# Kernel tuning notes

Hardware: AMD Instinct MI355X
Metric: run time of the kernel (lower is better)

The kernel has to match this reference:

```python
import jax, jax.numpy as jnp
import numpy as np

TAU = 1.1      # LIF membrane time constant
ALPHA = 4.0    # sigmoid surrogate sharpness (spikingjelly default)
EPS = 1e-5     # BatchNorm eps
SCALE = 0.125  # attention scale


def lif(x, v_th):
    # Single-step LIF, v init 0, decay_input=True: v = x / tau; spike = H(v - v_th)
    # Straight-through: forward heaviside, backward sigmoid surrogate derivative.
    u = x / TAU - v_th
    sg = jax.nn.sigmoid(ALPHA * u)
    return sg + jax.lax.stop_gradient((u >= 0.0).astype(x.dtype) - sg)


def bn(x, gamma, beta):
    # BatchNorm1d in training mode on [B, C, N]: stats over (B, N) per channel
    mean = jnp.mean(x, axis=(0, 2), keepdims=True)
    var = jnp.var(x, axis=(0, 2), keepdims=True)
    return gamma[None, :, None] * (x - mean) * jax.lax.rsqrt(var + EPS) + beta[None, :, None]


def conv1x1(w, x):
    # Conv1d kernel_size=1: pointwise channel mix, x: [B,C,N], w: [O,C]
    return jnp.einsum('oc,bcn->bon', w, x)


def setup_inputs() -> dict:
    key = jax.random.key(0)
    B, C, N = 32, 512, 1024
    ks = jax.random.split(key, 6)
    s = 1.0 / np.sqrt(C)
    inp = {"x": jax.random.normal(ks[0], (B, C, N), jnp.float32)}
    for name, k in zip(["q", "k", "v", "proj"], ks[1:5]):
        inp[name + "_w"] = jax.random.uniform(k, (C, C), jnp.float32, -s, s)
        inp[name + "_gamma"] = jnp.ones((C,), jnp.float32)
        inp[name + "_beta"] = jnp.zeros((C,), jnp.float32)
    inp["proj_b"] = jax.random.uniform(ks[5], (C,), jnp.float32, -s, s)
    return inp


def reference(x, q_w, q_gamma, q_beta, k_w, k_gamma, k_beta, v_w, v_gamma, v_beta,
              proj_w, proj_b, proj_gamma, proj_beta):
    # x: [B, C, N]
    q = lif(bn(conv1x1(q_w, x), q_gamma, q_beta), 1.0)  # [B,C,N] spikes
    k = lif(bn(conv1x1(k_w, x), k_gamma, k_beta), 1.0)
    v = lif(bn(conv1x1(v_w, x), v_gamma, v_beta), 1.0)
    # linear (softmax-free) attention: kv[c,d] = sum_n k[n,c] v[n,d]
    kv = jnp.einsum('bcn,bdn->bcd', k, v)               # [B,C,C]
    attn = jnp.einsum('bcn,bcd->bdn', q, kv) * SCALE    # [B,C,N] (already transposed back)
    attn = lif(attn, 0.5)
    out = conv1x1(proj_w, attn) + proj_b[None, :, None]
    return lif(bn(out, proj_gamma, proj_beta), 1.0)
```

## Files before the change

kernel.cpp:

```cpp
#include <hip/hip_runtime.h>
#include <cstddef>


#define CC 512
#define BB 32
#define NN 1024

typedef __attribute__((ext_vector_type(4))) float v4f;
typedef __attribute__((ext_vector_type(2))) float v2f;
typedef __attribute__((ext_vector_type(4))) int v4i;
typedef __attribute__((ext_vector_type(8))) int v8i;
typedef unsigned char uchar;
typedef unsigned long long ull;

__device__ __forceinline__ uchar f2e4s(float v) {
  const uchar s = (v < 0.f) ? 0x80 : 0x00;
  float a = fabsf(v);
  if (a >= 464.f) return s | 0x7E;
  if (a < 0.015625f) {
    int q = (int)rintf(a * 512.f);
    return s | (uchar)q;
  }
  const int e = (int)((__float_as_uint(a) >> 23) & 0xFF) - 126;
  const float scale = __uint_as_float((unsigned)(4 - e + 127) << 23);
  const int q = (int)rintf(a * scale);
  int code = ((e - 1 + 7) << 3) + (q - 8);
  if (code > 0x7E) code = 0x7E;
  return s | (uchar)code;
}
__device__ __forceinline__ float e42f(uchar b) {
  const int e = (b >> 3) & 15, m = b & 7;
  const float mag = e ? __uint_as_float((unsigned)((e + 120) << 23) | ((unsigned)m << 20))
                      : (float)m * 0.001953125f;
  return (b & 0x80) ? -mag : mag;
}

__device__ __forceinline__ unsigned pk4_fp8(float a0, float a1, float a2, float a3) {
#if __has_builtin(__builtin_amdgcn_cvt_pk_fp8_f32)
  int r = __builtin_amdgcn_cvt_pk_fp8_f32(a0, a1, 0, false);
  r = __builtin_amdgcn_cvt_pk_fp8_f32(a2, a3, r, true);
  return (unsigned)r;
#else
  return (unsigned)f2e4s(a0) | ((unsigned)f2e4s(a1) << 8) |
         ((unsigned)f2e4s(a2) << 16) | ((unsigned)f2e4s(a3) << 24);
#endif
}
__device__ __forceinline__ uchar enc1(float v) {
#if __has_builtin(__builtin_amdgcn_cvt_pk_fp8_f32)
  return (uchar)(__builtin_amdgcn_cvt_pk_fp8_f32(v, v, 0, false) & 0xFF);
#else
  return f2e4s(v);
#endif
}
template <bool HI>
__device__ __forceinline__ v2f dec2(int src) {
#if __has_builtin(__builtin_amdgcn_cvt_pk_f32_fp8)
  return __builtin_amdgcn_cvt_pk_f32_fp8(src, HI);
#else
  v2f r;
  const int s = HI ? (src >> 16) : src;
  r[0] = e42f((uchar)s);
  r[1] = e42f((uchar)(s >> 8));
  return r;
#endif
}

__device__ __forceinline__ void gload16(const void* g, void* l) {
  __builtin_amdgcn_global_load_lds(
      (const __attribute__((address_space(1))) unsigned int*)g,
      (__attribute__((address_space(3))) unsigned int*)l, 16, 0, 0);
}

__device__ __forceinline__ float2 chan_affine(const float* __restrict__ P, int c,
                                              float g, float bt) {
  const float* pc = P + (size_t)c * 16;
  float S = 0.f, Q = 0.f;
#pragma unroll
  for (int t = 0; t < 8; t++) { S += pc[2 * t]; Q += pc[2 * t + 1]; }
  const float mean = S * (1.f / 32768.f);
  const float var = fmaxf(Q * (1.f / 32768.f) - mean * mean, 0.f);
  const float rinv = 1.f / sqrtf(var + 1e-5f);
  const float a = g * rinv;
  return make_float2(a, bt - mean * a);
}

template <int EPI>
__global__ __launch_bounds__(256) void gemm8(const uchar* __restrict__ A,
                                             const uchar* __restrict__ B,
                                             uchar* __restrict__ Cout,
                                             const float* __restrict__ bias,
                                             int M, int N, int K,
                                             long sA, long sB, long sC) {
  __shared__ __align__(16) uchar lds[32768];
  const int b = blockIdx.z;
  const uchar* Ab = A + (size_t)b * sA;
  const uchar* Bb = B + (size_t)b * sB;
  const int m0 = blockIdx.y * 128, n0 = blockIdx.x * 128;
  const int tid = threadIdx.x;
  const int wave = tid >> 6, lane = tid & 63;
  const int lrow = lane & 15, lquad = lane >> 4;
  const int wr = wave >> 1, wc = wave & 1;

  v4f acc[4][4];
#pragma unroll
  for (int i = 0; i < 4; i++)
#pragma unroll
    for (int j = 0; j < 4; j++) acc[i][j] = (v4f)0.f;

  const uchar* gA0 = Ab + (size_t)(m0 + 32 * wave + lrow) * K + lquad * 32;
  const uchar* gA1 = gA0 + (size_t)16 * K;
  const uchar* gB0 = Bb + (size_t)(n0 + 32 * wave + lrow) * K + lquad * 32;
  const uchar* gB1 = gB0 + (size_t)16 * K;
  uchar* lA0 = lds + (2 * wave) * 2048;
  uchar* lA1 = lA0 + 2048;
  uchar* lB0 = lds + 16384 + (2 * wave) * 2048;
  uchar* lB1 = lB0 + 2048;

  for (int k0 = 0; k0 < K; k0 += 128) {
    gload16(gA0, lA0);
    gload16(gA0 + 16, lA0 + 1024);
    gload16(gA1, lA1);
    gload16(gA1 + 16, lA1 + 1024);
    gload16(gB0, lB0);
    gload16(gB0 + 16, lB0 + 1024);
    gload16(gB1, lB1);
    gload16(gB1 + 16, lB1 + 1024);
    gA0 += 128; gA1 += 128; gB0 += 128; gB1 += 128;
    __syncthreads();
    const uchar* ra = lds + (size_t)(4 * wr) * 2048 + 16 * lane;
    const uchar* rb = lds + 16384 + (size_t)(4 * wc) * 2048 + 16 * lane;
    v8i af[4], bf[4];
#pragma unroll
    for (int i = 0; i < 4; i++) {
      const v4i lo = *(const v4i*)(ra + i * 2048);
      const v4i hi = *(const v4i*)(ra + i * 2048 + 1024);
      af[i][0] = lo[0]; af[i][1] = lo[1]; af[i][2] = lo[2]; af[i][3] = lo[3];
      af[i][4] = hi[0]; af[i][5] = hi[1]; af[i][6] = hi[2]; af[i][7] = hi[3];
    }
#pragma unroll
    for (int j = 0; j < 4; j++) {
      const v4i lo = *(const v4i*)(rb + j * 2048);
      const v4i hi = *(const v4i*)(rb + j * 2048 + 1024);
      bf[j][0] = lo[0]; bf[j][1] = lo[1]; bf[j][2] = lo[2]; bf[j][3] = lo[3];
      bf[j][4] = hi[0]; bf[j][5] = hi[1]; bf[j][6] = hi[2]; bf[j][7] = hi[3];
    }
#pragma unroll
    for (int i = 0; i < 4; i++)
#pragma unroll
      for (int j = 0; j < 4; j++)
        acc[i][j] = __builtin_amdgcn_mfma_scale_f32_16x16x128_f8f6f4(
            af[i], bf[j], acc[i][j], 0, 0, 0, 127, 0, 127);
    __syncthreads();
  }

  if (EPI == 3) {
#pragma unroll
    for (int mi = 0; mi < 4; mi++)
#pragma unroll
      for (int r = 0; r < 4; r++) {
        const float bi = bias[m0 + 64 * wr + 16 * mi + lquad * 4 + r];
#pragma unroll
        for (int ni = 0; ni < 4; ni++) acc[mi][ni][r] += bi;
      }
  }

#pragma unroll
  for (int mi = 0; mi < 4; mi++) {
    const int row0 = m0 + 64 * wr + 16 * mi + lquad * 4;
#pragma unroll
    for (int ni = 0; ni < 4; ni++) {
      const int col = n0 + 64 * wc + 16 * ni + lrow;
      uchar* cp = Cout + (size_t)b * sC + (size_t)row0 * N + col;
      if (EPI == 1) {
#pragma unroll
        for (int r = 0; r < 4; r++) {
          const float u = (acc[mi][ni][r] * 0.125f) / 1.1f - 0.5f;
          cp[(size_t)r * N] = (u >= 0.f) ? (uchar)0x38 : (uchar)0;
        }
      } else {
        const unsigned pk = pk4_fp8(acc[mi][ni][0], acc[mi][ni][1],
                                    acc[mi][ni][2], acc[mi][ni][3]);
#pragma unroll
        for (int r = 0; r < 4; r++) cp[(size_t)r * N] = (uchar)(pk >> (8 * r));
      }
    }
  }
}

template <int EPI>
__global__ __launch_bounds__(512, 2) void gemm8p(const uchar* __restrict__ A,
                                                 const uchar* __restrict__ B,
                                                 uchar* __restrict__ Cout,
                                                 const float* __restrict__ bias,
                                                 int M, int N, int K,
                                                 long sA, long sB, long sC) {
  __shared__ __align__(16) uchar lds[131072];
  const int b = blockIdx.z;
  const uchar* Ab = A + (size_t)b * sA;
  const uchar* Bb = B + (size_t)b * sB;
  const int m0 = blockIdx.y * 256, n0 = blockIdx.x * 256;
  const int tid = threadIdx.x;
  const int wave = tid >> 6, lane = tid & 63;
  const int lrow = lane & 15, lquad = lane >> 4;
  const int wr = wave >> 2, wc = wave & 3;

  v4f acc[8][4];
#pragma unroll
  for (int i = 0; i < 8; i++)
#pragma unroll
    for (int j = 0; j < 4; j++) acc[i][j] = (v4f)0.f;

  const uchar* gA0 = Ab + (size_t)(m0 + 32 * wave + lrow) * K + lquad * 32;
  const uchar* gA1 = gA0 + (size_t)16 * K;
  const uchar* gB0 = Bb + (size_t)(n0 + 32 * wave + lrow) * K + lquad * 32;
  const uchar* gB1 = gB0 + (size_t)16 * K;

  const int NT = K >> 7;

  auto stage = [&](int bufi) {
    uchar* la = lds + bufi * 65536 + (2 * wave) * 2048;
    uchar* lb = la + 32768;
    gload16(gA0, la);
    gload16(gA0 + 16, la + 1024);
    gload16(gA1, la + 2048);
    gload16(gA1 + 16, la + 3072);
    gload16(gB0, lb);
    gload16(gB0 + 16, lb + 1024);
    gload16(gB1, lb + 2048);
    gload16(gB1 + 16, lb + 3072);
    gA0 += 128; gA1 += 128; gB0 += 128; gB1 += 128;
  };

  stage(0);
  if (NT > 1) stage(1);

  for (int kt = 0; kt < NT; ++kt) {
    const int cur = kt & 1;
    if (kt + 1 < NT) {
      asm volatile("s_waitcnt vmcnt(8)" ::: "memory");
    } else {
      asm volatile("s_waitcnt vmcnt(0)" ::: "memory");
    }
    __builtin_amdgcn_s_barrier();

    const uchar* raA = lds + cur * 65536 + (size_t)(8 * wr) * 2048 + 16 * lane;
    const uchar* raB = lds + cur * 65536 + 32768 + (size_t)(4 * wc) * 2048 + 16 * lane;
    v8i bf[4];
#pragma unroll
    for (int j = 0; j < 4; ++j) {
      const v4i lo = *(const v4i*)(raB + j * 2048);
      const v4i hi = *(const v4i*)(raB + j * 2048 + 1024);
      bf[j][0] = lo[0]; bf[j][1] = lo[1]; bf[j][2] = lo[2]; bf[j][3] = lo[3];
      bf[j][4] = hi[0]; bf[j][5] = hi[1]; bf[j][6] = hi[2]; bf[j][7] = hi[3];
    }
#pragma unroll
    for (int p = 0; p < 4; ++p) {
      const uchar* ra = raA + (size_t)(2 * p) * 2048;
      const v4i a0lo = *(const v4i*)(ra);
      const v4i a0hi = *(const v4i*)(ra + 1024);
      const v4i a1lo = *(const v4i*)(ra + 2048);
      const v4i a1hi = *(const v4i*)(ra + 3072);
      __builtin_amdgcn_s_barrier();
      asm volatile("s_waitcnt lgkmcnt(0)" ::: "memory");
      __builtin_amdgcn_sched_barrier(0);
      v8i af0, af1;
      af0[0] = a0lo[0]; af0[1] = a0lo[1]; af0[2] = a0lo[2]; af0[3] = a0lo[3];
      af0[4] = a0hi[0]; af0[5] = a0hi[1]; af0[6] = a0hi[2]; af0[7] = a0hi[3];
      af1[0] = a1lo[0]; af1[1] = a1lo[1]; af1[2] = a1lo[2]; af1[3] = a1lo[3];
      af1[4] = a1hi[0]; af1[5] = a1hi[1]; af1[6] = a1hi[2]; af1[7] = a1hi[3];
      __builtin_amdgcn_s_setprio(1);
#pragma unroll
      for (int j = 0; j < 4; ++j) {
        acc[2 * p][j] = __builtin_amdgcn_mfma_scale_f32_16x16x128_f8f6f4(
            af0, bf[j], acc[2 * p][j], 0, 0, 0, 127, 0, 127);
        acc[2 * p + 1][j] = __builtin_amdgcn_mfma_scale_f32_16x16x128_f8f6f4(
            af1, bf[j], acc[2 * p + 1][j], 0, 0, 0, 127, 0, 127);
      }
      __builtin_amdgcn_s_setprio(0);
      __builtin_amdgcn_s_barrier();
    }

    if (kt + 2 < NT) {
      stage(cur);
    }
  }

  if (EPI == 3) {
#pragma unroll
    for (int mi = 0; mi < 8; mi++)
#pragma unroll
      for (int r = 0; r < 4; r++) {
        const float bi = bias[m0 + 128 * wr + 16 * mi + lquad * 4 + r];
#pragma unroll
        for (int ni = 0; ni < 4; ni++) acc[mi][ni][r] += bi;
      }
  }

#pragma unroll
  for (int mi = 0; mi < 8; mi++) {
    const int row0 = m0 + 128 * wr + 16 * mi + lquad * 4;
#pragma unroll
    for (int ni = 0; ni < 4; ni++) {
      const int col = n0 + 64 * wc + 16 * ni + lrow;
      uchar* cp = Cout + (size_t)b * sC + (size_t)row0 * N + col;
      if (EPI == 1) {
#pragma unroll
        for (int r = 0; r < 4; r++) {
          const float u = (acc[mi][ni][r] * 0.125f) / 1.1f - 0.5f;
          cp[(size_t)r * N] = (u >= 0.f) ? (uchar)0x38 : (uchar)0;
        }
      } else {
        const unsigned pk = pk4_fp8(acc[mi][ni][0], acc[mi][ni][1],
                                    acc[mi][ni][2], acc[mi][ni][3]);
#pragma unroll
        for (int r = 0; r < 4; r++) cp[(size_t)r * N] = (uchar)(pk >> (8 * r));
      }
    }
  }
}

__global__ __launch_bounds__(256) void stats_part8_k(const uchar* __restrict__ in,
                                                     float* __restrict__ P,
                                                     long bstride) {
  const int part = blockIdx.x, c = blockIdx.y;
  const int tid = threadIdx.x;
  const int bi = part * 4 + (tid >> 6);
  const int lane = tid & 63;
  const uchar* p = in + (size_t)bi * bstride + (size_t)c * 1024 + lane * 16;
  const uint4 u = *(const uint4*)p;
  const int w4[4] = {(int)u.x, (int)u.y, (int)u.z, (int)u.w};
  float s = 0.f, s2 = 0.f;
#pragma unroll
  for (int t = 0; t < 4; t++) {
    const v2f a = dec2<false>(w4[t]);
    const v2f bb = dec2<true>(w4[t]);
    s += (a[0] + a[1]) + (bb[0] + bb[1]);
    s2 += a[0] * a[0] + a[1] * a[1] + bb[0] * bb[0] + bb[1] * bb[1];
  }
#pragma unroll
  for (int off = 32; off > 0; off >>= 1) {
    s += __shfl_down(s, off, 64);
    s2 += __shfl_down(s2, off, 64);
  }
  __shared__ float rs[4], rq[4];
  const int w = tid >> 6;
  if (lane == 0) { rs[w] = s; rq[w] = s2; }
  __syncthreads();
  if (tid == 0) {
    float2 o = make_float2(rs[0] + rs[1] + rs[2] + rs[3],
                           rq[0] + rq[1] + rq[2] + rq[3]);
    *(float2*)(P + (size_t)(c * 8 + part) * 2) = o;
  }
}

__global__ __launch_bounds__(256) void apply_all_k(const uchar* __restrict__ qkv8,
                                                   uchar* __restrict__ q8,
                                                   uchar* __restrict__ k8,
                                                   uchar* __restrict__ v8,
                                                   const float* __restrict__ P,
                                                   const float* __restrict__ qg, const float* __restrict__ qb,
                                                   const float* __restrict__ kg, const float* __restrict__ kb,
                                                   const float* __restrict__ vg, const float* __restrict__ vb) {
  const int bid = blockIdx.x;
  const int tid = threadIdx.x;
  if (bid < 16384) {
    __shared__ uchar tile[32][33];
    const int nb = bid & 31, cb = (bid >> 5) & 15, b = bid >> 9;
    const int n0 = nb * 32, c0 = cb * 32;
    const uchar* in = qkv8 + (size_t)b * (1536 * 1024);
    const int cl = tid >> 3;
    const int n4 = (tid & 7) * 4;
    const int c = c0 + cl;
    const float2 ab = chan_affine(P, c, qg[c], qb[c]);
    const unsigned w = *(const unsigned*)(in + (size_t)c * 1024 + n0 + n4);
    const v2f a = dec2<false>((int)w);
    const v2f bb = dec2<true>((int)w);
    tile[cl][n4 + 0] = (ab.x * a[0] + ab.y >= 1.1f) ? (uchar)0x38 : (uchar)0;
    tile[cl][n4 + 1] = (ab.x * a[1] + ab.y >= 1.1f) ? (uchar)0x38 : (uchar)0;
    tile[cl][n4 + 2] = (ab.x * bb[0] + ab.y >= 1.1f) ? (uchar)0x38 : (uchar)0;
    tile[cl][n4 + 3] = (ab.x * bb[1] + ab.y >= 1.1f) ? (uchar)0x38 : (uchar)0;
    __syncthreads();
    uchar* out = q8 + (size_t)b * (NN * CC);
    const int nl = tid >> 3;
    const int cq = (tid & 7) * 4;
    uchar4 v;
    v.x = tile[cq][nl]; v.y = tile[cq + 1][nl];
    v.z = tile[cq + 2][nl]; v.w = tile[cq + 3][nl];
    *(uchar4*)(out + (size_t)(n0 + nl) * CC + c0 + cq) = v;
  } else {
    const int t0 = bid - 16384;
    const int sec = t0 >> 13;
    const int blk = t0 & 8191;
    const size_t t = (size_t)blk * 256 + tid;
    const size_t i = t * 8;
    const int b = (int)(i >> 19);
    const int rem = (int)(i & 524287);
    const int c = rem >> 10, n = rem & 1023;
    const int cg = 512 + 512 * sec + c;
    const float2 ab = chan_affine(P, cg, sec ? vg[c] : kg[c], sec ? vb[c] : kb[c]);
    const uchar* src = qkv8 + (size_t)b * (1536 * 1024) + (size_t)cg * 1024 + n;
    const uint2 u = *(const uint2*)src;
    ull packed = 0;
    {
      const v2f a = dec2<false>((int)u.x);
      const v2f bb = dec2<true>((int)u.x);
      const float f[4] = {a[0], a[1], bb[0], bb[1]};
#pragma unroll
      for (int j = 0; j < 4; j++)
        packed |= ((ab.x * f[j] + ab.y >= 1.1f) ? 0x38ull : 0ull) << (8 * j);
    }
    {
      const v2f a = dec2<false>((int)u.y);
      const v2f bb = dec2<true>((int)u.y);
      const float f[4] = {a[0], a[1], bb[0], bb[1]};
#pragma unroll
      for (int j = 0; j < 4; j++)
        packed |= ((ab.x * f[j] + ab.y >= 1.1f) ? 0x38ull : 0ull) << (8 * (4 + j));
    }
    uchar* dst = (sec ? v8 : k8) + (size_t)b * (CC * NN) + (size_t)c * 1024 + n;
    *(ull*)dst = packed;
  }
}

__global__ __launch_bounds__(256) void apply_final_k(const uchar* __restrict__ in,
                                                     float* __restrict__ outp,
                                                     const float* __restrict__ Pp,
                                                     const float* __restrict__ pg,
                                                     const float* __restrict__ pb) {
  const size_t idx = ((size_t)blockIdx.x * 256 + threadIdx.x) * 8;
  const int c = (int)((idx >> 10) & (CC - 1));
  const float2 ab = chan_affine(Pp, c, pg[c], pb[c]);
  const uint2 u = *(const uint2*)(in + idx);
  float of[8];
  {
    const v2f a = dec2<false>((int)u.x);
    const v2f bb = dec2<true>((int)u.x);
    of[0] = (ab.x * a[0] + ab.y >= 1.1f) ? 1.f : 0.f;
    of[1] = (ab.x * a[1] + ab.y >= 1.1f) ? 1.f : 0.f;
    of[2] = (ab.x * bb[0] + ab.y >= 1.1f) ? 1.f : 0.f;
    of[3] = (ab.x * bb[1] + ab.y >= 1.1f) ? 1.f : 0.f;
  }
  {
    const v2f a = dec2<false>((int)u.y);
    const v2f bb = dec2<true>((int)u.y);
    of[4] = (ab.x * a[0] + ab.y >= 1.1f) ? 1.f : 0.f;
    of[5] = (ab.x * a[1] + ab.y >= 1.1f) ? 1.f : 0.f;
    of[6] = (ab.x * bb[0] + ab.y >= 1.1f) ? 1.f : 0.f;
    of[7] = (ab.x * bb[1] + ab.y >= 1.1f) ? 1.f : 0.f;
  }
  float* op = outp + idx;
  *(float4*)op = make_float4(of[0], of[1], of[2], of[3]);
  *(float4*)(op + 4) = make_float4(of[4], of[5], of[6], of[7]);
}

__global__ __launch_bounds__(256) void prep_k(const float* __restrict__ x,
                                              const float* __restrict__ w0, const float* __restrict__ w1,
                                              const float* __restrict__ w2, const float* __restrict__ w3,
                                              uchar* __restrict__ xT8,
                                              uchar* __restrict__ o0, uchar* __restrict__ o1,
                                              uchar* __restrict__ o2, uchar* __restrict__ o3) {
  const int bid = blockIdx.x;
  const int tid = threadIdx.x;
  if (bid < 16384) {
    __shared__ uchar tile[32][33];
    const int nb = bid & 31, cb = (bid >> 5) & 15, b = bid >> 9;
    const int n0 = nb * 32, c0 = cb * 32;
    const float* in = x + (size_t)b * (CC * NN);
    const int tx = tid & 31, ty = tid >> 5;
#pragma unroll
    for (int i = 0; i < 32; i += 8) {
      tile[ty + i][tx] = enc1(in[(size_t)(c0 + ty + i) * NN + n0 + tx]);
    }
    __syncthreads();
    uchar* o = xT8 + (size_t)b * (NN * CC);
    const int nl = tid >> 3;
    const int cq = (tid & 7) * 4;
    uchar4 v;
    v.x = tile[cq][nl]; v.y = tile[cq + 1][nl];
    v.z = tile[cq + 2][nl]; v.w = tile[cq + 3][nl];
    *(uchar4*)(o + (size_t)(n0 + nl) * CC + c0 + cq) = v;
  } else {
    const int t = bid - 16384;
    const int mat = t >> 8, blk = t & 255;
    const float* src = (mat == 0) ? w0 : (mat == 1) ? w1 : (mat == 2) ? w2 : w3;
    uchar* dst = (mat == 0) ? o0 : (mat == 1) ? o1 : (mat == 2) ? o2 : o3;
    const int i = (blk * 256 + tid) * 4;
    float4 v = *(const float4*)(src + i);
    *(unsigned*)(dst + i) = pk4_fp8(v.x, v.y, v.z, v.w);
  }
}

extern "C" void kernel_launch(void* const* d_in, const int* in_sizes, int n_in,
                              void* d_out, int out_size, void* d_ws, size_t ws_size,
                              hipStream_t stream) {
  const float* x          = (const float*)d_in[0];
  const float* q_w        = (const float*)d_in[1];
  const float* q_gamma    = (const float*)d_in[2];
  const float* q_beta     = (const float*)d_in[3];
  const float* k_w        = (const float*)d_in[4];
  const float* k_gamma    = (const float*)d_in[5];
  const float* k_beta     = (const float*)d_in[6];
  const float* v_w        = (const float*)d_in[7];
  const float* v_gamma    = (const float*)d_in[8];
  const float* v_beta     = (const float*)d_in[9];
  const float* proj_w     = (const float*)d_in[10];
  const float* proj_gamma = (const float*)d_in[11];
  const float* proj_beta  = (const float*)d_in[12];
  const float* proj_b     = (const float*)d_in[13];

  char* base = (char*)d_ws;
  const size_t MB = 1u << 20;
  uchar*  xT8    = (uchar*)base;
  uchar*  qkv8   = (uchar*)(base + 16 * MB);
  uchar*  q8     = (uchar*)(base + 64 * MB);
  uchar*  k8     = (uchar*)(base + 80 * MB);
  uchar*  v8     = (uchar*)(base + 96 * MB);
  uchar*  kvT8   = (uchar*)(base + 112 * MB);
  uchar*  attnT8 = (uchar*)(base + 120 * MB);
  uchar*  outpre8= (uchar*)(base + 136 * MB);
  uchar*  wqkv8  = (uchar*)(base + 152 * MB);
  uchar*  wp8    = wqkv8 + 3 * CC * CC;
  float*  P      = (float*)(base + 154 * MB);
  float*  Pp     = P + 1536 * 16;
  float* dout = (float*)d_out;

  const long QKVL = (long)3 * CC * NN;
  const long NCL  = (long)NN * CC;
  const long CNL  = (long)CC * NN;
  const long KVL  = (long)CC * CC;

  prep_k<<<17408, 256, 0, stream>>>(x, q_w, k_w, v_w, proj_w, xT8,
                                    wqkv8, wqkv8 + CC * CC, wqkv8 + 2 * CC * CC, wp8);

  gemm8p<2><<<dim3(NN / 256, 1536 / 256, BB), 512, 0, stream>>>(
      wqkv8, xT8, qkv8, nullptr, 1536, NN, CC, 0, NCL, QKVL);

  stats_part8_k<<<dim3(8, 1536), 256, 0, stream>>>(qkv8, P, QKVL);

  apply_all_k<<<32768, 256, 0, stream>>>(qkv8, q8, k8, v8, P,
                                         q_gamma, q_beta, k_gamma, k_beta,
                                         v_gamma, v_beta);

  gemm8<0><<<dim3(CC / 128, CC / 128, BB), 256, 0, stream>>>(
      v8, k8, kvT8, nullptr, CC, CC, NN, CNL, CNL, KVL);
  gemm8p<1><<<dim3(CC / 256, NN / 256, BB), 512, 0, stream>>>(
      q8, kvT8, attnT8, nullptr, NN, CC, CC, NCL, KVL, NCL);
  gemm8p<3><<<dim3(NN / 256, CC / 256, BB), 512, 0, stream>>>(
      wp8, attnT8, outpre8, proj_b, CC, NN, CC, 0, NCL, CNL);

  stats_part8_k<<<dim3(8, CC), 256, 0, stream>>>(outpre8, Pp, CNL);
  apply_final_k<<<8192, 256, 0, stream>>>(outpre8, dout, Pp, proj_gamma, proj_beta);
}
```

Baseline: 300.5 us.

## Double-buffer LDS in kv GEMM with async prefetch and MFMA priority

Converts the 128x128 fp8 GEMM used for the k·v product into a double-buffered pipeline. The next K-tile's global-to-LDS loads are issued while the current tile is computed, using vmcnt waits and raw barriers in place of two __syncthreads per iteration. It also raises wave priority around the MFMA block. LDS use doubles to 64KB, which may reduce blocks per CU, and the code relies on the vmcnt(8) counting matching the eight loads per stage.

New measurement: 302.5 us. Within noise of the previous version (+0.7%).

```diff
diff --git a/kernel.cpp b/kernel.cpp
--- a/kernel.cpp
+++ b/kernel.cpp
@@ -85,13 +85,13 @@
 }
 
 template <int EPI>
-__global__ __launch_bounds__(256) void gemm8(const uchar* __restrict__ A,
-                                             const uchar* __restrict__ B,
-                                             uchar* __restrict__ Cout,
-                                             const float* __restrict__ bias,
-                                             int M, int N, int K,
-                                             long sA, long sB, long sC) {
-  __shared__ __align__(16) uchar lds[32768];
+__global__ __launch_bounds__(256) void gemm8q(const uchar* __restrict__ A,
+                                              const uchar* __restrict__ B,
+                                              uchar* __restrict__ Cout,
+                                              const float* __restrict__ bias,
+                                              int M, int N, int K,
+                                              long sA, long sB, long sC) {
+  __shared__ __align__(16) uchar lds[65536];
   const int b = blockIdx.z;
   const uchar* Ab = A + (size_t)b * sA;
   const uchar* Bb = B + (size_t)b * sB;
@@ -111,24 +111,37 @@
   const uchar* gA1 = gA0 + (size_t)16 * K;
   const uchar* gB0 = Bb + (size_t)(n0 + 32 * wave + lrow) * K + lquad * 32;
   const uchar* gB1 = gB0 + (size_t)16 * K;
-  uchar* lA0 = lds + (2 * wave) * 2048;
-  uchar* lA1 = lA0 + 2048;
-  uchar* lB0 = lds + 16384 + (2 * wave) * 2048;
-  uchar* lB1 = lB0 + 2048;
-
-  for (int k0 = 0; k0 < K; k0 += 128) {
-    gload16(gA0, lA0);
-    gload16(gA0 + 16, lA0 + 1024);
-    gload16(gA1, lA1);
-    gload16(gA1 + 16, lA1 + 1024);
-    gload16(gB0, lB0);
-    gload16(gB0 + 16, lB0 + 1024);
-    gload16(gB1, lB1);
-    gload16(gB1 + 16, lB1 + 1024);
+
+  const int NT = K >> 7;
+
+  auto stage = [&](int bufi) {
+    uchar* la = lds + bufi * 32768 + (2 * wave) * 2048;
+    uchar* lb = la + 16384;
+    gload16(gA0, la);
+    gload16(gA0 + 16, la + 1024);
+    gload16(gA1, la + 2048);
+    gload16(gA1 + 16, la + 3072);
+    gload16(gB0, lb);
+    gload16(gB0 + 16, lb + 1024);
+    gload16(gB1, lb + 2048);
+    gload16(gB1 + 16, lb + 3072);
     gA0 += 128; gA1 += 128; gB0 += 128; gB1 += 128;
-    __syncthreads();
-    const uchar* ra = lds + (size_t)(4 * wr) * 2048 + 16 * lane;
-    const uchar* rb = lds + 16384 + (size_t)(4 * wc) * 2048 + 16 * lane;
+  };
+
+  stage(0);
+  if (NT > 1) stage(1);
+
+  for (int kt = 0; kt < NT; ++kt) {
+    const int cur = kt & 1;
+    if (kt + 1 < NT) {
+      asm volatile("s_waitcnt vmcnt(8)" ::: "memory");
+    } else {
+      asm volatile("s_waitcnt vmcnt(0)" ::: "memory");
+    }
+    __builtin_amdgcn_s_barrier();
+
+    const uchar* ra = lds + cur * 32768 + (size_t)(4 * wr) * 2048 + 16 * lane;
+    const uchar* rb = lds + cur * 32768 + 16384 + (size_t)(4 * wc) * 2048 + 16 * lane;
     v8i af[4], bf[4];
 #pragma unroll
     for (int i = 0; i < 4; i++) {
@@ -144,13 +157,19 @@
       bf[j][0] = lo[0]; bf[j][1] = lo[1]; bf[j][2] = lo[2]; bf[j][3] = lo[3];
       bf[j][4] = hi[0]; bf[j][5] = hi[1]; bf[j][6] = hi[2]; bf[j][7] = hi[3];
     }
+    __builtin_amdgcn_s_setprio(1);
 #pragma unroll
     for (int i = 0; i < 4; i++)
 #pragma unroll
       for (int j = 0; j < 4; j++)
         acc[i][j] = __builtin_amdgcn_mfma_scale_f32_16x16x128_f8f6f4(
             af[i], bf[j], acc[i][j], 0, 0, 0, 127, 0, 127);
-    __syncthreads();
+    __builtin_amdgcn_s_setprio(0);
+
+    if (kt + 2 < NT) {
+      __builtin_amdgcn_s_barrier();
+      stage(cur);
+    }
   }
 
   if (EPI == 3) {
@@ -541,7 +560,7 @@
                                          q_gamma, q_beta, k_gamma, k_beta,
                                          v_gamma, v_beta);
 
-  gemm8<0><<<dim3(CC / 128, CC / 128, BB), 256, 0, stream>>>(
+  gemm8q<0><<<dim3(CC / 128, CC / 128, BB), 256, 0, stream>>>(
       v8, k8, kvT8, nullptr, CC, CC, NN, CNL, CNL, KVL);
   gemm8p<1><<<dim3(CC / 256, NN / 256, BB), 512, 0, stream>>>(
       q8, kvT8, attnT8, nullptr, NN, CC, CC, NCL, KVL, NCL);
```
